# Performance work log

Hardware: AMD Instinct MI355X
Metric: run time of the kernel (lower is better)

## Reference

```python
import jax, jax.numpy as jnp
import numpy as np

H = 768
L = 9
M = 5            # max_span_length
CTX_RATIO = 0.5
NEG_INF = -1e30


def setup_inputs() -> dict:
    key = jax.random.key(0)
    ks = jax.random.split(key, 12)
    B, S = 4, 2048
    sc = 1.0 / np.sqrt(H)
    return {
        "sequence_output": jax.random.normal(ks[0], (B, S, H), dtype=jnp.float32),
        "Wc": jax.random.normal(ks[1], (H, L), dtype=jnp.float32) * sc,
        "bc": jnp.zeros((L,), dtype=jnp.float32),
        "wa": jax.random.normal(ks[2], (H,), dtype=jnp.float32) * sc,
        "ba": jnp.zeros((), dtype=jnp.float32),
        "W1": jax.random.normal(ks[3], (2 * H, H), dtype=jnp.float32) * (1.0 / np.sqrt(2 * H)),
        "b1": jnp.zeros((H,), dtype=jnp.float32),
        "gamma": jnp.ones((H,), dtype=jnp.float32),
        "beta": jnp.zeros((H,), dtype=jnp.float32),
        "W2": jax.random.normal(ks[4], (H, L), dtype=jnp.float32) * sc,
        "b2": jnp.zeros((L,), dtype=jnp.float32),
    }


def reference(sequence_output, Wc, bc, wa, ba, W1, b1, gamma, beta, W2, b2):
    x = sequence_output                        # [B,S,H]
    B, S, _ = x.shape
    base_logits = jnp.einsum('bsh,hl->bsl', x, Wc) + bc   # [B,S,L]

    # sliding-window indices: window [i-M, i+M] clipped to [0, S)
    offsets = jnp.arange(-M, M + 1)            # [W]
    idx = jnp.arange(S)[:, None] + offsets     # [S,W]
    valid = (idx >= 0) & (idx < S)             # [S,W]
    idx_c = jnp.clip(idx, 0, S - 1)            # [S,W]

    # attention scores over window (span_attention linear -> scalar per token)
    scores = jnp.einsum('bsh,h->bs', x, wa) + ba           # [B,S]
    win_scores = scores[:, idx_c]                          # [B,S,W]
    win_scores = jnp.where(valid[None], win_scores, NEG_INF)
    attn = jax.nn.softmax(win_scores, axis=-1)             # [B,S,W]

    win_tokens = x[:, idx_c]                               # [B,S,W,H] gather
    weighted_ctx = jnp.einsum('bsw,bswh->bsh', attn, win_tokens)

    token_with_ctx = jnp.concatenate([x, weighted_ctx], axis=-1)  # [B,S,2H]
    h = jnp.einsum('bsd,dh->bsh', token_with_ctx, W1) + b1
    # LayerNorm (eps = 1e-5, torch default)
    mu = jnp.mean(h, axis=-1, keepdims=True)
    var = jnp.mean((h - mu) ** 2, axis=-1, keepdims=True)
    h = (h - mu) * jax.lax.rsqrt(var + 1e-5) * gamma + beta
    h = jax.nn.gelu(h, approximate=False)                  # torch nn.GELU default (erf)
    ctx_logits = jnp.einsum('bsh,hl->bsl', h, W2) + b2

    return (1.0 - CTX_RATIO) * base_logits + CTX_RATIO * ctx_logits
```

## Files before the change

kernel.cpp:

```cpp
#include <hip/hip_runtime.h>
#include <hip/hip_bf16.h>
#include <math.h>

#define S_LEN 2048
#define BATCH 4
#define HDIM 768
#define LOUT 9
#define NROWS (BATCH*S_LEN)
#define K2H 1536
#define WIN 11
#define NEG_INF_F (-1e30f)

typedef __attribute__((ext_vector_type(4))) float f32x4;
typedef __attribute__((ext_vector_type(8))) short bf16x8;

static __device__ __forceinline__ void async_ld16(const void* g, void* l) {
  __builtin_amdgcn_global_load_lds((const __attribute__((address_space(1))) void*)g,
                                   (__attribute__((address_space(3))) void*)l, 16, 0, 0);
}

static __device__ __forceinline__ unsigned short f2bf(float f) {
  union { float f; unsigned int u; } v; v.f = f;
  unsigned int u = v.u;
  unsigned int r = (u + 0x7fffu + ((u >> 16) & 1u)) >> 16;
  return (unsigned short)r;
}

static __device__ __forceinline__ float bf2f(unsigned short h) {
  union { unsigned int u; float f; } v; v.u = ((unsigned int)h) << 16;
  return v.f;
}

__global__ __launch_bounds__(256) void k_prep_w1t(const float* __restrict__ W1,
                                                  unsigned short* __restrict__ W1t) {
  __shared__ float tile[32][33];
  int bk = blockIdx.x % 48;
  int bn = blockIdx.x / 48;
  int tc = threadIdx.x % 32;
  int tr = threadIdx.x / 32;
  #pragma unroll
  for (int i = 0; i < 32; i += 8) {
    tile[tr + i][tc] = W1[(bk*32 + tr + i) * HDIM + bn*32 + tc];
  }
  __syncthreads();
  #pragma unroll
  for (int i = 0; i < 32; i += 8) {
    W1t[(bn*32 + tr + i) * K2H + bk*32 + tc] = f2bf(tile[tc][tr + i]);
  }
}

__global__ __launch_bounds__(192) void k_prep(const float* __restrict__ x,
                                              const float* __restrict__ wa,
                                              const float* __restrict__ ba,
                                              const float* __restrict__ Wc,
                                              const float* __restrict__ bc,
                                              unsigned short* __restrict__ xc,
                                              float* __restrict__ scores,
                                              float* __restrict__ base) {
  __shared__ float red[3][LOUT + 1];
  int bid = blockIdx.x;
  int row = (bid & 7) * 1024 + (bid >> 3);
  int t = threadIdx.x;
  int lane = t & 63, wave = t >> 6;
  const float4 v = *(const float4*)(x + row * HDIM + t * 4);
  const float4 w = *(const float4*)(wa + t * 4);
  ushort4 o;
  o.x = f2bf(v.x); o.y = f2bf(v.y); o.z = f2bf(v.z); o.w = f2bf(v.w);
  *(ushort4*)(xc + row * K2H + t * 4) = o;

  float pv[LOUT + 1];
  pv[LOUT] = v.x * w.x + v.y * w.y + v.z * w.z + v.w * w.w;
  #pragma unroll
  for (int l = 0; l < LOUT; ++l) pv[l] = 0.f;
  const float xvv[4] = { v.x, v.y, v.z, v.w };
  #pragma unroll
  for (int j = 0; j < 4; ++j) {
    const float* wr = Wc + (t * 4 + j) * LOUT;
    #pragma unroll
    for (int l = 0; l < LOUT; ++l) pv[l] += xvv[j] * wr[l];
  }
  #pragma unroll
  for (int l = 0; l <= LOUT; ++l)
    #pragma unroll
    for (int m = 1; m < 64; m <<= 1) pv[l] += __shfl_xor(pv[l], m);
  if (lane == 0) {
    #pragma unroll
    for (int l = 0; l <= LOUT; ++l) red[wave][l] = pv[l];
  }
  __syncthreads();
  if (t < LOUT) {
    base[row * LOUT + t] = red[0][t] + red[1][t] + red[2][t] + bc[t];
  } else if (t == LOUT) {
    scores[row] = red[0][LOUT] + red[1][LOUT] + red[2][LOUT] + ba[0];
  }
}

__global__ __launch_bounds__(192) void k_ctx(const float* __restrict__ scores,
                                             unsigned short* __restrict__ xc) {
  __shared__ float swin[WIN];
  int bid = blockIdx.x;
  int row = (bid & 7) * 1024 + (bid >> 3);
  int b = row >> 11, s = row & 2047;
  int t = threadIdx.x;
  if (t < WIN) {
    int j = s - 5 + t;
    bool valid = (j >= 0) && (j < S_LEN);
    int jc = valid ? j : (j < 0 ? 0 : S_LEN - 1);
    swin[t] = valid ? scores[b * S_LEN + jc] : NEG_INF_F;
  }
  __syncthreads();
  float mx = swin[0];
  #pragma unroll
  for (int w = 1; w < WIN; ++w) mx = fmaxf(mx, swin[w]);
  float es[WIN], ssum = 0.f;
  #pragma unroll
  for (int w = 0; w < WIN; ++w) {
    float sv = swin[w];
    es[w] = (sv > -1e29f) ? __expf(sv - mx) : 0.f;
    ssum += es[w];
  }
  float inv = 1.f / ssum;
  float c0 = 0.f, c1 = 0.f, c2 = 0.f, c3 = 0.f;
  #pragma unroll
  for (int w = 0; w < WIN; ++w) {
    float aw = es[w] * inv;
    int j = s - 5 + w;
    int jc = (j < 0) ? 0 : ((j >= S_LEN) ? S_LEN - 1 : j);
    const ushort4 uv = *(const ushort4*)(xc + (((long)b * S_LEN + jc) * K2H) + t * 4);
    c0 += aw * bf2f(uv.x);
    c1 += aw * bf2f(uv.y);
    c2 += aw * bf2f(uv.z);
    c3 += aw * bf2f(uv.w);
  }
  ushort4 o;
  o.x = f2bf(c0); o.y = f2bf(c1); o.z = f2bf(c2); o.w = f2bf(c3);
  *(ushort4*)(xc + row * K2H + HDIM + t * 4) = o;
}

__global__ __launch_bounds__(256, 4) void k_gemm(const unsigned short* __restrict__ A,
                                                 const unsigned short* __restrict__ Bt,
                                                 const float* __restrict__ b1,
                                                 float* __restrict__ Hout) {
  __shared__ unsigned short As[2][128 * 32];
  __shared__ unsigned short Bs[2][64 * 32];
  int bid = blockIdx.x;
  int obid = (bid & 7) * 96 + (bid >> 3);
  int bm = obid / 12, bn = obid % 12;
  int t = threadIdx.x;
  int lane = t & 63, wave = t >> 6;

  int fl = ((lane >> 2) ^ (lane >> 4)) & 3;
  int sSrc = ((lane & 3) ^ fl);
  int rIn = lane >> 2;

  const unsigned short* gA = A  + (bm * 128 + wave * 32 + rIn) * K2H + sSrc * 8;
  const unsigned short* gB = Bt + (bn * 64  + wave * 16 + rIn) * K2H + sSrc * 8;

  f32x4 acc[2][4] = {};

  int laneRow = lane & 15;
  int slot = lane >> 4;
  int fr = ((lane & 3) ^ ((lane >> 2) & 3));
  int rdOff = ((slot ^ fr) & 3) * 8;

#define STAGE(buf, kt) do {                                                    \
    async_ld16(gA + (kt),             &As[buf][(wave * 32) * 32]);             \
    async_ld16(gA + 16 * K2H + (kt),  &As[buf][(wave * 32 + 16) * 32]);        \
    async_ld16(gB + (kt),             &Bs[buf][(wave * 16) * 32]);             \
  } while (0)

#define COMPUTE(buf) do {                                                      \
    bf16x8 af[2], bfv[4];                                                      \
    _Pragma("unroll")                                                          \
    for (int m = 0; m < 2; ++m)                                                \
      af[m] = *(const bf16x8*)(&As[buf][(wave * 32 + m * 16 + laneRow) * 32 + rdOff]); \
    _Pragma("unroll")                                                          \
    for (int n = 0; n < 4; ++n)                                                \
      bfv[n] = *(const bf16x8*)(&Bs[buf][(n * 16 + laneRow) * 32 + rdOff]);    \
    _Pragma("unroll")                                                          \
    for (int m = 0; m < 2; ++m)                                                \
      _Pragma("unroll")                                                        \
      for (int n = 0; n < 4; ++n)                                              \
        acc[m][n] = __builtin_amdgcn_mfma_f32_16x16x32_bf16(af[m], bfv[n], acc[m][n], 0, 0, 0); \
  } while (0)

  STAGE(0, 0);
  __syncthreads();
  int cur = 0;
  for (int kt = 32; kt < K2H; kt += 32) {
    STAGE(cur ^ 1, kt);
    COMPUTE(cur);
    __syncthreads();
    cur ^= 1;
  }
  COMPUTE(cur);

  int orow = bm * 128 + wave * 32 + (lane >> 4) * 4;
  int ocol = bn * 64 + (lane & 15);
  #pragma unroll
  for (int m = 0; m < 2; ++m)
    #pragma unroll
    for (int n = 0; n < 4; ++n) {
      int col = ocol + n * 16;
      float bv = b1[col];
      #pragma unroll
      for (int r = 0; r < 4; ++r) {
        Hout[(orow + m * 16 + r) * HDIM + col] = acc[m][n][r] + bv;
      }
    }
#undef STAGE
#undef COMPUTE
}

__global__ __launch_bounds__(256) void k_ln(const float* __restrict__ Hin,
                                            const float* __restrict__ gamma,
                                            const float* __restrict__ beta,
                                            const float* __restrict__ W2,
                                            const float* __restrict__ b2,
                                            const float* __restrict__ base,
                                            float* __restrict__ out) {
  __shared__ float redS[4], redQ[4], redp[4][LOUT];
  int row = blockIdx.x;
  int t = threadIdx.x;
  int lane = t & 63, wave = t >> 6;
  const float* hr = Hin + row * HDIM;
  float v0 = hr[t], v1 = hr[t + 256], v2 = hr[t + 512];
  float s1 = v0 + v1 + v2;
  float s2 = v0 * v0 + v1 * v1 + v2 * v2;
  #pragma unroll
  for (int m = 1; m < 64; m <<= 1) { s1 += __shfl_xor(s1, m); s2 += __shfl_xor(s2, m); }
  if (lane == 0) { redS[wave] = s1; redQ[wave] = s2; }
  __syncthreads();
  s1 = redS[0] + redS[1] + redS[2] + redS[3];
  s2 = redQ[0] + redQ[1] + redQ[2] + redQ[3];
  float mu = s1 * (1.f / HDIM);
  float var = s2 * (1.f / HDIM) - mu * mu;
  float rstd = rsqrtf(var + 1e-5f);
  float p[LOUT] = {};
  float vv[3] = { v0, v1, v2 };
  #pragma unroll
  for (int i = 0; i < 3; ++i) {
    int e = t + i * 256;
    float g = (vv[i] - mu) * rstd * gamma[e] + beta[e];
    float gg = 0.5f * g * (1.f + erff(g * 0.70710678118654752f));
    const float* wrow = W2 + e * LOUT;
    #pragma unroll
    for (int l = 0; l < LOUT; ++l) p[l] += gg * wrow[l];
  }
  #pragma unroll
  for (int l = 0; l < LOUT; ++l)
    #pragma unroll
    for (int m = 1; m < 64; m <<= 1) p[l] += __shfl_xor(p[l], m);
  if (lane == 0) {
    #pragma unroll
    for (int l = 0; l < LOUT; ++l) redp[wave][l] = p[l];
  }
  __syncthreads();
  if (t < LOUT) {
    float cl = redp[0][t] + redp[1][t] + redp[2][t] + redp[3][t] + b2[t];
    out[row * LOUT + t] = 0.5f * base[row * LOUT + t] + 0.5f * cl;
  }
}

extern "C" void kernel_launch(void* const* d_in, const int* in_sizes, int n_in,
                              void* d_out, int out_size, void* d_ws, size_t ws_size,
                              hipStream_t stream) {
  const float* x     = (const float*)d_in[0];
  const float* Wc    = (const float*)d_in[1];
  const float* bc    = (const float*)d_in[2];
  const float* wa    = (const float*)d_in[3];
  const float* ba    = (const float*)d_in[4];
  const float* W1    = (const float*)d_in[5];
  const float* b1    = (const float*)d_in[6];
  const float* gamma = (const float*)d_in[7];
  const float* beta  = (const float*)d_in[8];
  const float* W2    = (const float*)d_in[9];
  const float* b2    = (const float*)d_in[10];
  float* out = (float*)d_out;

  char* ws = (char*)d_ws;
  unsigned short* xc  = (unsigned short*)(ws);
  unsigned short* w1t = (unsigned short*)(ws + 25165824);
  float* scores       = (float*)(ws + 27525120);
  float* base         = (float*)(ws + 27557888);
  float* hbuf         = (float*)(ws + 27852800);

  k_prep_w1t<<<dim3(1152), dim3(256), 0, stream>>>(W1, w1t);
  k_prep    <<<dim3(8192), dim3(192), 0, stream>>>(x, wa, ba, Wc, bc, xc, scores, base);
  k_ctx     <<<dim3(8192), dim3(192), 0, stream>>>(scores, xc);
  k_gemm    <<<dim3(768),  dim3(256), 0, stream>>>(xc, w1t, b1, hbuf);
  k_ln      <<<dim3(8192), dim3(256), 0, stream>>>(hbuf, gamma, beta, W2, b2, base, out);
}
```

Before: 183.5 us.

## Deepen GEMM pipeline to four LDS stages and vectorize LayerNorm loads

The GEMM main loop moves from a double buffer with __syncthreads to a four-stage ring of async global-to-LDS loads. It waits with explicit vmcnt counters plus s_barrier, and raises wave priority around the MFMA block. This is meant to hide global load latency better, at the cost of more LDS and a lower launch-bounds occupancy hint (3 instead of 4). The LayerNorm/GELU/W2 kernel now uses 192 threads with float4 loads of the hidden row, gamma and beta, so memory transactions are wider and the reduction has fewer waves.

Result: faster. 179.2 us (-2.3%).

```diff
diff --git a/kernel.cpp b/kernel.cpp
--- a/kernel.cpp
+++ b/kernel.cpp
@@ -137,12 +137,12 @@
   *(ushort4*)(xc + row * K2H + HDIM + t * 4) = o;
 }
 
-__global__ __launch_bounds__(256, 4) void k_gemm(const unsigned short* __restrict__ A,
+__global__ __launch_bounds__(256, 3) void k_gemm(const unsigned short* __restrict__ A,
                                                  const unsigned short* __restrict__ Bt,
                                                  const float* __restrict__ b1,
                                                  float* __restrict__ Hout) {
-  __shared__ unsigned short As[2][128 * 32];
-  __shared__ unsigned short Bs[2][64 * 32];
+  __shared__ unsigned short As[4][128 * 32];
+  __shared__ unsigned short Bs[4][64 * 32];
   int bid = blockIdx.x;
   int obid = (bid & 7) * 96 + (bid >> 3);
   int bm = obid / 12, bn = obid % 12;
@@ -177,23 +177,29 @@
     _Pragma("unroll")                                                          \
     for (int n = 0; n < 4; ++n)                                                \
       bfv[n] = *(const bf16x8*)(&Bs[buf][(n * 16 + laneRow) * 32 + rdOff]);    \
+    __builtin_amdgcn_s_setprio(1);                                             \
     _Pragma("unroll")                                                          \
     for (int m = 0; m < 2; ++m)                                                \
       _Pragma("unroll")                                                        \
       for (int n = 0; n < 4; ++n)                                              \
         acc[m][n] = __builtin_amdgcn_mfma_f32_16x16x32_bf16(af[m], bfv[n], acc[m][n], 0, 0, 0); \
+    __builtin_amdgcn_s_setprio(0);                                             \
   } while (0)
 
+#define WBAR(n) asm volatile("s_waitcnt vmcnt(" #n ")\n\ts_barrier" ::: "memory")
+
   STAGE(0, 0);
-  __syncthreads();
-  int cur = 0;
-  for (int kt = 32; kt < K2H; kt += 32) {
-    STAGE(cur ^ 1, kt);
-    COMPUTE(cur);
-    __syncthreads();
-    cur ^= 1;
-  }
-  COMPUTE(cur);
+  STAGE(1, 32);
+  STAGE(2, 64);
+
+  for (int tt = 0; tt < 45; ++tt) {
+    WBAR(6);
+    STAGE((tt + 3) & 3, (tt + 3) * 32);
+    COMPUTE(tt & 3);
+  }
+  WBAR(6);  COMPUTE(1);
+  WBAR(3);  COMPUTE(2);
+  WBAR(0);  COMPUTE(3);
 
   int orow = bm * 128 + wave * 32 + (lane >> 4) * 4;
   int ocol = bn * 64 + (lane & 15);
@@ -210,40 +216,43 @@
     }
 #undef STAGE
 #undef COMPUTE
-}
-
-__global__ __launch_bounds__(256) void k_ln(const float* __restrict__ Hin,
+#undef WBAR
+}
+
+__global__ __launch_bounds__(192) void k_ln(const float* __restrict__ Hin,
                                             const float* __restrict__ gamma,
                                             const float* __restrict__ beta,
                                             const float* __restrict__ W2,
                                             const float* __restrict__ b2,
                                             const float* __restrict__ base,
                                             float* __restrict__ out) {
-  __shared__ float redS[4], redQ[4], redp[4][LOUT];
+  __shared__ float redS[3], redQ[3], redp[3][LOUT];
   int row = blockIdx.x;
   int t = threadIdx.x;
   int lane = t & 63, wave = t >> 6;
-  const float* hr = Hin + row * HDIM;
-  float v0 = hr[t], v1 = hr[t + 256], v2 = hr[t + 512];
-  float s1 = v0 + v1 + v2;
-  float s2 = v0 * v0 + v1 * v1 + v2 * v2;
+  const float4 v = *(const float4*)(Hin + row * HDIM + t * 4);
+  float s1 = v.x + v.y + v.z + v.w;
+  float s2 = v.x*v.x + v.y*v.y + v.z*v.z + v.w*v.w;
   #pragma unroll
   for (int m = 1; m < 64; m <<= 1) { s1 += __shfl_xor(s1, m); s2 += __shfl_xor(s2, m); }
   if (lane == 0) { redS[wave] = s1; redQ[wave] = s2; }
   __syncthreads();
-  s1 = redS[0] + redS[1] + redS[2] + redS[3];
-  s2 = redQ[0] + redQ[1] + redQ[2] + redQ[3];
+  s1 = redS[0] + redS[1] + redS[2];
+  s2 = redQ[0] + redQ[1] + redQ[2];
   float mu = s1 * (1.f / HDIM);
   float var = s2 * (1.f / HDIM) - mu * mu;
   float rstd = rsqrtf(var + 1e-5f);
+  const float4 g4 = *(const float4*)(gamma + t * 4);
+  const float4 be4 = *(const float4*)(beta + t * 4);
   float p[LOUT] = {};
-  float vv[3] = { v0, v1, v2 };
-  #pragma unroll
-  for (int i = 0; i < 3; ++i) {
-    int e = t + i * 256;
-    float g = (vv[i] - mu) * rstd * gamma[e] + beta[e];
+  const float vv[4] = { v.x, v.y, v.z, v.w };
+  const float gv[4] = { g4.x, g4.y, g4.z, g4.w };
+  const float bv[4] = { be4.x, be4.y, be4.z, be4.w };
+  #pragma unroll
+  for (int j = 0; j < 4; ++j) {
+    float g = (vv[j] - mu) * rstd * gv[j] + bv[j];
     float gg = 0.5f * g * (1.f + erff(g * 0.70710678118654752f));
-    const float* wrow = W2 + e * LOUT;
+    const float* wrow = W2 + (t * 4 + j) * LOUT;
     #pragma unroll
     for (int l = 0; l < LOUT; ++l) p[l] += gg * wrow[l];
   }
@@ -257,7 +266,7 @@
   }
   __syncthreads();
   if (t < LOUT) {
-    float cl = redp[0][t] + redp[1][t] + redp[2][t] + redp[3][t] + b2[t];
+    float cl = redp[0][t] + redp[1][t] + redp[2][t] + b2[t];
     out[row * LOUT + t] = 0.5f * base[row * LOUT + t] + 0.5f * cl;
   }
 }
@@ -289,5 +298,5 @@
   k_prep    <<<dim3(8192), dim3(192), 0, stream>>>(x, wa, ba, Wc, bc, xc, scores, base);
   k_ctx     <<<dim3(8192), dim3(192), 0, stream>>>(scores, xc);
   k_gemm    <<<dim3(768),  dim3(256), 0, stream>>>(xc, w1t, b1, hbuf);
-  k_ln      <<<dim3(8192), dim3(256), 0, stream>>>(hbuf, gamma, beta, W2, b2, base, out);
-}
+  k_ln      <<<dim3(8192), dim3(192), 0, stream>>>(hbuf, gamma, beta, W2, b2, base, out);
+}
```
